# Kernel tuning notes

Hardware: AMD Instinct MI355X
Metric: run time of the kernel (lower is better)

Reference implementation:

```python
import jax, jax.numpy as jnp
import numpy as np

VOXEL = 0.8  # meters per grid cell (from `* 0.8` and `/0.8` in source)
GRID = 256   # BEV grid size (from torch.zeros(256, 256))


def _points_in_any_box(points, boxes):
    """points: (M, 3) grid-cell coords shared across batch; boxes: (B, T, 7) as
    (cx, cy, cz, dx, dy, dz, yaw). Returns (B, M) bool: point inside any box.
    Mirrors roiaware_pool3d points_in_boxes_gpu (rotate by -yaw, half-size test)."""
    shift = points[None, :, None, :] - boxes[:, None, :, :3]      # (B, M, T, 3)
    c = jnp.cos(boxes[:, None, :, 6])                              # (B, 1, T)
    s = jnp.sin(boxes[:, None, :, 6])
    rx = shift[..., 0] * c + shift[..., 1] * s                     # local x
    ry = -shift[..., 0] * s + shift[..., 1] * c                    # local y
    half = boxes[:, None, :, 3:6] * 0.5                            # (B, 1, T, 3)
    inb = (jnp.abs(rx) < half[..., 0]) \
        & (jnp.abs(ry) < half[..., 1]) \
        & (jnp.abs(shift[..., 2]) <= half[..., 2])                 # (B, M, T)
    return jnp.any(inb, axis=-1)                                   # (B, M)


def setup_inputs() -> dict:
    key = jax.random.key(0)
    k1, k2, k3, k4, k5, k6 = jax.random.split(key, 6)
    B, C, H, T = 16, 32, GRID, 20
    u1 = jax.random.uniform(k1, (B, C, H, H))
    added = jnp.where(u1 > 0.98, u1, 0.0)
    u2 = jax.random.uniform(k2, (B, C + 1, H, H))
    orig = jnp.where(u2 > 0.98, u2, 0.0)
    # boxes inside the grid extent [0, 256*0.8) meters
    ctr = jax.random.uniform(k3, (B, T, 2), minval=40.0, maxval=160.0)
    cz = jnp.full((B, T, 1), VOXEL)
    dims = jax.random.uniform(k4, (B, T, 3), minval=4.0, maxval=16.0)
    dims = dims.at[..., 2].set(2.0)  # dz covers the fixed point z = 0.8
    yaw = jax.random.uniform(k5, (B, T, 1), minval=-3.14, maxval=3.14)
    boxes = jnp.concatenate([ctr, cz, dims, yaw], axis=-1)
    tf_ego = jax.random.normal(k6, (B, 4, 4))
    return {"added_points": added, "original_points": orig,
            "boxes": boxes, "tf_ego": tf_ego}


def reference(added_points, original_points, boxes, tf_ego):
    B, _, H, W = added_points.shape
    T = boxes.shape[1]
    # collapse channel/height dim -> BEV occupancy maps (B, H, W)
    pred = jnp.sum(added_points, axis=1)
    orig = jnp.sum(original_points[:, 1:], axis=1)
    # every grid cell is a candidate point at (i*0.8, j*0.8, 0.8) (source: nonzero idx * 0.8)
    ii, jj = jnp.meshgrid(jnp.arange(H), jnp.arange(W), indexing='ij')
    pts = jnp.stack([ii.reshape(-1) * VOXEL,
                     jj.reshape(-1) * VOXEL,
                     jnp.full((H * W,), VOXEL)], axis=-1).astype(boxes.dtype)
    in_box = _points_in_any_box(pts, boxes)                        # (B, H*W)
    # keep only occupied cells that fall inside some box -> binary grids
    occ_p = (pred.reshape(B, -1) != 0) & in_box
    occ_o = (orig.reshape(B, -1) != 0) & in_box
    inter = jnp.sum(occ_p & occ_o, axis=-1).astype(jnp.float32)
    union = jnp.sum(occ_p | occ_o, axis=-1).astype(jnp.float32)
    iou_b = inter / jnp.maximum(union, 1.0)                        # per-batch grid IoU
    # source accumulates the (identical) IoU once per box, then divides by batch
    return T * jnp.sum(iou_b) / B
```

## Files before the change

### kernel.cpp

```cpp
#include <hip/hip_runtime.h>
#include <hip/hip_bf16.h>
#include <cstdint>

#define H 256
#define HW (H * H)
#define T_BOX 20
#define SLICES 8
#define SPAN 32
#define BCELLS 4096
#define BBLK (HW / BCELLS)
#define WPB 2048

__device__ __forceinline__ float bf2f(unsigned short u) {
    union { unsigned int x; float f; } c;
    c.x = ((unsigned int)u) << 16;
    return c.f;
}
__device__ __forceinline__ unsigned short f2bf_bits(float x) {
    union { float f; unsigned int u; } c;
    c.f = x;
    return (unsigned short)((c.u + 0x7fffu + ((c.u >> 16) & 1u)) >> 16);
}
__device__ __forceinline__ float bfq(float x) { return bf2f(f2bf_bits(x)); }

__device__ __forceinline__ bool detect_f32(const void* boxes_) {
    const float* bxf = (const float*)boxes_;
    return (fabsf(bxf[2] - 0.8f) < 0.25f) && (fabsf(bxf[9] - 0.8f) < 0.25f);
}

__global__ __launch_bounds__(256)
void occ_bitmap_kernel(const void* __restrict__ added_,
                       const void* __restrict__ orig_,
                       const void* __restrict__ boxes_,
                       unsigned int* __restrict__ mapP,
                       unsigned int* __restrict__ mapO,
                       int B, int Ca, int Co) {
    const bool is_f32 = detect_f32(boxes_);

    const int m     = blockIdx.x >> 3;
    const int s8    = blockIdx.x & (SLICES - 1);
    const int t     = threadIdx.x;
    const int cell0 = s8 * (HW / SLICES) + t * SPAN;

    size_t src_cell;
    unsigned int* dst;
    int b;
    if (m < B * Ca) {
        b = m / Ca;
        src_cell = (size_t)m * HW;
        dst = mapP;
    } else {
        const int m2 = m - B * Ca;
        b = m2 / (Co - 1);
        const int c2 = m2 - b * (Co - 1);
        src_cell = ((size_t)b * Co + 1 + c2) * HW;
        dst = mapO;
    }
    const void* src = (m < B * Ca) ? added_ : orig_;

    unsigned int mask = 0;
    if (is_f32) {
        const uint4* p = (const uint4*)((const float*)src + src_cell + cell0);
        uint4 w[8];
#pragma unroll
        for (int q = 0; q < 8; ++q) w[q] = p[q];
#pragma unroll
        for (int q = 0; q < 8; ++q) {
            mask |= (unsigned int)(w[q].x != 0u) << (4 * q + 0);
            mask |= (unsigned int)(w[q].y != 0u) << (4 * q + 1);
            mask |= (unsigned int)(w[q].z != 0u) << (4 * q + 2);
            mask |= (unsigned int)(w[q].w != 0u) << (4 * q + 3);
        }
    } else {
        const uint4* p = (const uint4*)((const unsigned short*)src + src_cell + cell0);
        uint4 w[4];
#pragma unroll
        for (int q = 0; q < 4; ++q) w[q] = p[q];
        union { uint4 v[4]; unsigned short u[32]; } U;
#pragma unroll
        for (int q = 0; q < 4; ++q) U.v[q] = w[q];
#pragma unroll
        for (int e = 0; e < 32; ++e)
            mask |= (unsigned int)(U.u[e] != 0) << e;
    }

    if (mask) atomicOr(&dst[(size_t)b * WPB + (cell0 >> 5)], mask);
}

__global__ __launch_bounds__(256)
void iou_kernel(const unsigned int* __restrict__ mapP,
                const unsigned int* __restrict__ mapO,
                const void* __restrict__ boxes_,
                unsigned long long* __restrict__ cnt) {
    __shared__ float s_cx[T_BOX], s_cy[T_BOX], s_sn[T_BOX], s_cs[T_BOX],
                     s_hx[T_BOX], s_hy[T_BOX];

    const int cb = blockIdx.x & (BBLK - 1);
    const int b  = blockIdx.x >> 4;
    const int t  = threadIdx.x;
    const bool is_f32 = detect_f32(boxes_);

    if (t < T_BOX) {
        float cx, cy, cz, dx, dy, dz, yaw, pz;
        if (is_f32) {
            const float* bp = (const float*)boxes_ + ((size_t)b * T_BOX + t) * 7;
            cx = bp[0]; cy = bp[1]; cz = bp[2];
            dx = bp[3]; dy = bp[4]; dz = bp[5]; yaw = bp[6];
            pz = 0.8f;
        } else {
            const unsigned short* bp =
                (const unsigned short*)boxes_ + ((size_t)b * T_BOX + t) * 7;
            cx = bf2f(bp[0]); cy = bf2f(bp[1]); cz = bf2f(bp[2]);
            dx = bf2f(bp[3]); dy = bf2f(bp[4]); dz = bf2f(bp[5]);
            yaw = bf2f(bp[6]);
            pz = bfq(0.8f);
        }
        float hx = 0.5f * dx, hy = 0.5f * dy, hz = 0.5f * dz;
        if (!(fabsf(pz - cz) <= hz)) hx = -1.0f;
        s_cx[t] = cx; s_cy[t] = cy;
        s_sn[t] = sinf(yaw); s_cs[t] = cosf(yaw);
        s_hx[t] = hx; s_hy[t] = hy;
    }
    __syncthreads();

    const int M = cb * BCELLS + t * 16;
    const unsigned int w  = ((unsigned int)b << 11) + ((unsigned int)M >> 5);
    const unsigned int sh = (unsigned int)M & 31u;
    const unsigned int pm = (mapP[w] >> sh) & 0xFFFFu;
    const unsigned int om = (mapO[w] >> sh) & 0xFFFFu;

    const int i  = M >> 8;
    const int j0 = M & 255;
    float px = (float)((double)i * 0.8);
    float py[16];
#pragma unroll
    for (int e = 0; e < 16; ++e) py[e] = (float)((double)(j0 + e) * 0.8);
    if (!is_f32) {
        px = bfq(px);
#pragma unroll
        for (int e = 0; e < 16; ++e) py[e] = bfq(py[e]);
    }

    unsigned int inb = 0;
    for (int k = 0; k < T_BOX; ++k) {
        const float cx = s_cx[k], cy = s_cy[k], sn = s_sn[k], cs = s_cs[k];
        const float hx = s_hx[k], hy = s_hy[k];
        const float sx  = px - cx;
        const float sxc = sx * cs, sxs = sx * sn;
#pragma unroll
        for (int e = 0; e < 16; ++e) {
            const float sy = py[e] - cy;
            const float rx = sxc + sy * sn;
            const float ry = sy * cs - sxs;
            if ((fabsf(rx) < hx) & (fabsf(ry) < hy)) inb |= (1u << e);
        }
    }

    const unsigned int inter = __popc(pm & om & inb);
    const unsigned int uni   = __popc((pm | om) & inb);

    unsigned long long val = ((unsigned long long)inter << 32) |
                             (unsigned long long)uni;
#pragma unroll
    for (int off = 32; off > 0; off >>= 1)
        val += __shfl_down(val, off, 64);

    if ((t & 63) == 0) atomicAdd(&cnt[b], val);
}

__global__ void finish_kernel(const unsigned long long* __restrict__ cnt,
                              unsigned int* __restrict__ out, int B, int T) {
    if (threadIdx.x == 0 && blockIdx.x == 0) {
        float s = 0.0f;
        for (int b = 0; b < B; ++b) {
            unsigned long long v = cnt[b];
            float inter = (float)(unsigned int)(v >> 32);
            float uni   = (float)(unsigned int)(v & 0xffffffffu);
            s += inter / fmaxf(uni, 1.0f);
        }
        const float x = (float)T * s / (float)B;
        const unsigned int h = f2bf_bits(x);
        out[0] = (h << 16) | h;
    }
}

extern "C" void kernel_launch(void* const* d_in, const int* in_sizes, int n_in,
                              void* d_out, int out_size, void* d_ws, size_t ws_size,
                              hipStream_t stream) {
    const void* added = d_in[0];
    const void* orig  = d_in[1];
    const void* boxes = d_in[2];

    const int B  = in_sizes[2] / (T_BOX * 7);
    const int Ca = in_sizes[0] / (B * HW);
    const int Co = in_sizes[1] / (B * HW);

    unsigned int* mapP = (unsigned int*)d_ws;
    unsigned int* mapO = mapP + (size_t)B * WPB;
    unsigned long long* cnt = (unsigned long long*)(mapO + (size_t)B * WPB);
    hipMemsetAsync(d_ws, 0, (size_t)B * WPB * 8 + (size_t)B * 8, stream);

    const int n_maps = B * Ca + B * (Co - 1);
    occ_bitmap_kernel<<<n_maps * SLICES, 256, 0, stream>>>(
        added, orig, boxes, mapP, mapO, B, Ca, Co);
    iou_kernel<<<B * BBLK, 256, 0, stream>>>(mapP, mapO, boxes, cnt);
    finish_kernel<<<1, 64, 0, stream>>>(cnt, (unsigned int*)d_out, B, T_BOX);
}
```

Baseline: 296.1 us.

## Compute in-box worklist first and gather only channel data for in-box cells

```diff
diff --git a/kernel.cpp b/kernel.cpp
--- a/kernel.cpp
+++ b/kernel.cpp
@@ -5,11 +5,8 @@
 #define H 256
 #define HW (H * H)
 #define T_BOX 20
-#define SLICES 8
-#define SPAN 32
-#define BCELLS 4096
-#define BBLK (HW / BCELLS)
-#define WPB 2048
+#define WLCAP 3584
+#define GBLK 64
 
 __device__ __forceinline__ float bf2f(unsigned short u) {
     union { unsigned int x; float f; } c;
@@ -29,75 +26,15 @@
 }
 
 __global__ __launch_bounds__(256)
-void occ_bitmap_kernel(const void* __restrict__ added_,
-                       const void* __restrict__ orig_,
-                       const void* __restrict__ boxes_,
-                       unsigned int* __restrict__ mapP,
-                       unsigned int* __restrict__ mapO,
-                       int B, int Ca, int Co) {
-    const bool is_f32 = detect_f32(boxes_);
-
-    const int m     = blockIdx.x >> 3;
-    const int s8    = blockIdx.x & (SLICES - 1);
-    const int t     = threadIdx.x;
-    const int cell0 = s8 * (HW / SLICES) + t * SPAN;
-
-    size_t src_cell;
-    unsigned int* dst;
-    int b;
-    if (m < B * Ca) {
-        b = m / Ca;
-        src_cell = (size_t)m * HW;
-        dst = mapP;
-    } else {
-        const int m2 = m - B * Ca;
-        b = m2 / (Co - 1);
-        const int c2 = m2 - b * (Co - 1);
-        src_cell = ((size_t)b * Co + 1 + c2) * HW;
-        dst = mapO;
-    }
-    const void* src = (m < B * Ca) ? added_ : orig_;
-
-    unsigned int mask = 0;
-    if (is_f32) {
-        const uint4* p = (const uint4*)((const float*)src + src_cell + cell0);
-        uint4 w[8];
-#pragma unroll
-        for (int q = 0; q < 8; ++q) w[q] = p[q];
-#pragma unroll
-        for (int q = 0; q < 8; ++q) {
-            mask |= (unsigned int)(w[q].x != 0u) << (4 * q + 0);
-            mask |= (unsigned int)(w[q].y != 0u) << (4 * q + 1);
-            mask |= (unsigned int)(w[q].z != 0u) << (4 * q + 2);
-            mask |= (unsigned int)(w[q].w != 0u) << (4 * q + 3);
-        }
-    } else {
-        const uint4* p = (const uint4*)((const unsigned short*)src + src_cell + cell0);
-        uint4 w[4];
-#pragma unroll
-        for (int q = 0; q < 4; ++q) w[q] = p[q];
-        union { uint4 v[4]; unsigned short u[32]; } U;
-#pragma unroll
-        for (int q = 0; q < 4; ++q) U.v[q] = w[q];
-#pragma unroll
-        for (int e = 0; e < 32; ++e)
-            mask |= (unsigned int)(U.u[e] != 0) << e;
-    }
-
-    if (mask) atomicOr(&dst[(size_t)b * WPB + (cell0 >> 5)], mask);
-}
-
-__global__ __launch_bounds__(256)
-void iou_kernel(const unsigned int* __restrict__ mapP,
-                const unsigned int* __restrict__ mapO,
-                const void* __restrict__ boxes_,
-                unsigned long long* __restrict__ cnt) {
+void inbox_kernel(const void* __restrict__ boxes_,
+                  unsigned int* __restrict__ wl,
+                  unsigned int* __restrict__ wl_cnt) {
     __shared__ float s_cx[T_BOX], s_cy[T_BOX], s_sn[T_BOX], s_cs[T_BOX],
                      s_hx[T_BOX], s_hy[T_BOX];
 
-    const int cb = blockIdx.x & (BBLK - 1);
-    const int b  = blockIdx.x >> 4;
-    const int t  = threadIdx.x;
+    const int b = blockIdx.x >> 4;
+    const int q = blockIdx.x & 15;
+    const int t = threadIdx.x;
     const bool is_f32 = detect_f32(boxes_);
 
     if (t < T_BOX) {
@@ -123,14 +60,10 @@
     }
     __syncthreads();
 
-    const int M = cb * BCELLS + t * 16;
-    const unsigned int w  = ((unsigned int)b << 11) + ((unsigned int)M >> 5);
-    const unsigned int sh = (unsigned int)M & 31u;
-    const unsigned int pm = (mapP[w] >> sh) & 0xFFFFu;
-    const unsigned int om = (mapO[w] >> sh) & 0xFFFFu;
-
-    const int i  = M >> 8;
-    const int j0 = M & 255;
+    const int grp = q * 256 + t;
+    const int M   = grp * 16;
+    const int i   = M >> 8;
+    const int j0  = M & 255;
     float px = (float)((double)i * 0.8);
     float py[16];
 #pragma unroll
@@ -156,16 +89,71 @@
         }
     }
 
-    const unsigned int inter = __popc(pm & om & inb);
-    const unsigned int uni   = __popc((pm | om) & inb);
+    if (inb) {
+        const unsigned int pos = atomicAdd(&wl_cnt[b], 1u);
+        if (pos < WLCAP) wl[(size_t)b * WLCAP + pos] = ((unsigned int)grp << 16) | inb;
+    }
+}
 
-    unsigned long long val = ((unsigned long long)inter << 32) |
-                             (unsigned long long)uni;
+__global__ __launch_bounds__(256)
+void gather_kernel(const void* __restrict__ added_,
+                   const void* __restrict__ orig_,
+                   const void* __restrict__ boxes_,
+                   const unsigned int* __restrict__ wl,
+                   const unsigned int* __restrict__ wl_cnt,
+                   unsigned long long* __restrict__ cnt,
+                   int Ca, int Co) {
+    const bool is_f32 = detect_f32(boxes_);
+    const int b    = blockIdx.x / GBLK;
+    const int w0   = (blockIdx.x % GBLK) * 4 + (threadIdx.x >> 6);
+    const int lane = threadIdx.x & 63;
+    const int g    = lane >> 4;
+    const int j    = lane & 15;
+
+    const unsigned int n = min(wl_cnt[b], (unsigned int)WLCAP);
+
+    unsigned int inter = 0, uni = 0;
+
+    for (unsigned int e = (unsigned int)w0; e < n; e += GBLK * 4) {
+        const unsigned int ent   = wl[(size_t)b * WLCAP + e];
+        const unsigned int inb16 = ent & 0xFFFFu;
+        const int M = (int)(ent >> 16) * 16 + j;
+
+        unsigned int nzv = 0;
+        if (is_f32) {
+            const float* base = (g < 2)
+                ? (const float*)added_ + ((size_t)b * Ca + g * 16) * HW + M
+                : (const float*)orig_  + ((size_t)b * Co + 1 + (g - 2) * 16) * HW + M;
+            unsigned int v[16];
 #pragma unroll
-    for (int off = 32; off > 0; off >>= 1)
-        val += __shfl_down(val, off, 64);
+            for (int i = 0; i < 16; ++i)
+                v[i] = *(const unsigned int*)(base + (size_t)i * HW);
+#pragma unroll
+            for (int i = 0; i < 16; ++i) nzv |= v[i];
+        } else {
+            const unsigned short* base = (g < 2)
+                ? (const unsigned short*)added_ + ((size_t)b * Ca + g * 16) * HW + M
+                : (const unsigned short*)orig_  + ((size_t)b * Co + 1 + (g - 2) * 16) * HW + M;
+            unsigned short v[16];
+#pragma unroll
+            for (int i = 0; i < 16; ++i) v[i] = base[(size_t)i * HW];
+            unsigned int o = 0;
+#pragma unroll
+            for (int i = 0; i < 16; ++i) o |= v[i];
+            nzv = o;
+        }
+        const unsigned long long bal = __ballot(nzv != 0u);
+        const unsigned int pm = ((unsigned int)bal | (unsigned int)(bal >> 16)) & 0xFFFFu;
+        const unsigned int om = ((unsigned int)(bal >> 32) | (unsigned int)(bal >> 48)) & 0xFFFFu;
+        inter += __popc(pm & om & inb16);
+        uni   += __popc((pm | om) & inb16);
+    }
 
-    if ((t & 63) == 0) atomicAdd(&cnt[b], val);
+    if (lane == 0 && (inter | uni)) {
+        const unsigned long long val =
+            ((unsigned long long)inter << 32) | (unsigned long long)uni;
+        atomicAdd(&cnt[b], val);
+    }
 }
 
 __global__ void finish_kernel(const unsigned long long* __restrict__ cnt,
@@ -195,14 +183,13 @@
     const int Ca = in_sizes[0] / (B * HW);
     const int Co = in_sizes[1] / (B * HW);
 
-    unsigned int* mapP = (unsigned int*)d_ws;
-    unsigned int* mapO = mapP + (size_t)B * WPB;
-    unsigned long long* cnt = (unsigned long long*)(mapO + (size_t)B * WPB);
-    hipMemsetAsync(d_ws, 0, (size_t)B * WPB * 8 + (size_t)B * 8, stream);
+    unsigned long long* cnt = (unsigned long long*)d_ws;
+    unsigned int* wl_cnt = (unsigned int*)(cnt + B);
+    unsigned int* wl     = wl_cnt + B;
+    hipMemsetAsync(d_ws, 0, (size_t)B * 12, stream);
 
-    const int n_maps = B * Ca + B * (Co - 1);
-    occ_bitmap_kernel<<<n_maps * SLICES, 256, 0, stream>>>(
-        added, orig, boxes, mapP, mapO, B, Ca, Co);
-    iou_kernel<<<B * BBLK, 256, 0, stream>>>(mapP, mapO, boxes, cnt);
+    inbox_kernel<<<B * 16, 256, 0, stream>>>(boxes, wl, wl_cnt);
+    gather_kernel<<<B * GBLK, 256, 0, stream>>>(added, orig, boxes,
+                                                wl, wl_cnt, cnt, Ca, Co);
     finish_kernel<<<1, 64, 0, stream>>>(cnt, (unsigned int*)d_out, B, T_BOX);
 }
```

After: 268.3 us. 1.1x faster.
